# Performance work log

Measured on AMD Instinct MI355X. Metric: run time of the kernel, lower is better.

## Reference

```python
import jax, jax.numpy as jnp
import numpy as np

B, S, W, D, T = 64, 512, 384, 768, 21


def setup_inputs() -> dict:
    key = jax.random.key(0)
    ks = jax.random.split(key, 8)
    hidden_states = jax.random.normal(ks[0], (B, S, D), dtype=jnp.float32)  # BERT last_hidden_state
    word_maps = jnp.sort(jax.random.randint(ks[1], (B, W), 0, S), axis=1)  # first-subword index per word
    tags = jax.random.randint(ks[2], (B, W), 0, T)
    word_mask = jnp.ones((B, W), dtype=bool)  # torchcrf requires mask[:,0] all on
    W_tag = jax.random.normal(ks[3], (T, D), dtype=jnp.float32) * 0.02  # hidden2tag weight
    b_tag = jnp.zeros((T,), dtype=jnp.float32)
    start_trans = jax.random.uniform(ks[4], (T,), minval=-0.1, maxval=0.1)
    end_trans = jax.random.uniform(ks[5], (T,), minval=-0.1, maxval=0.1)
    trans = jax.random.uniform(ks[6], (T, T), minval=-0.1, maxval=0.1)
    return dict(hidden_states=hidden_states, W_tag=W_tag, b_tag=b_tag,
                start_trans=start_trans, end_trans=end_trans, trans=trans,
                word_maps=word_maps, tags=tags, word_mask=word_mask)


def reference(hidden_states, W_tag, b_tag, start_trans, end_trans, trans,
              word_maps, tags, word_mask):
    # --- ragged subword -> word gather (vectorized form of the python loop) ---
    word_feats = jnp.take_along_axis(hidden_states, word_maps[:, :, None], axis=1)  # [B,W,D]
    # dropout is identity in eval / deterministic reference
    emissions = jnp.einsum('bwd,td->bwt', word_feats, W_tag) + b_tag  # [B,W,T]

    maskf = word_mask.astype(emissions.dtype)
    bidx = jnp.arange(tags.shape[0])

    # --- CRF numerator: score of the given tag sequence ---
    emit_sc = jnp.take_along_axis(emissions, tags[:, :, None], axis=2)[..., 0]  # [B,W]
    trans_sc = trans[tags[:, :-1], tags[:, 1:]]                                  # [B,W-1]
    num = start_trans[tags[:, 0]] + emit_sc[:, 0]
    num = num + jnp.sum((trans_sc + emit_sc[:, 1:]) * maskf[:, 1:], axis=1)
    lengths = word_mask.sum(axis=1)
    last_tags = jnp.take_along_axis(tags, (lengths - 1)[:, None], axis=1)[:, 0]
    num = num + end_trans[last_tags]

    # --- CRF denominator: log partition via forward recurrence (scan over time) ---
    def step(score, xm):
        em_t, m_t = xm  # [B,T], [B]
        nxt = jax.nn.logsumexp(score[:, :, None] + trans[None, :, :] + em_t[:, None, :], axis=1)
        return jnp.where(m_t[:, None], nxt, score), None

    score0 = start_trans[None, :] + emissions[:, 0]  # [B,T]
    score, _ = jax.lax.scan(step, score0,
                            (jnp.swapaxes(emissions[:, 1:], 0, 1), word_mask[:, 1:].T))
    log_z = jax.nn.logsumexp(score + end_trans[None, :], axis=1)  # [B]

    llh = num - log_z
    return -jnp.mean(llh)  # reduction='mean', negated
```

## Files before the change

kernel.cpp:

```cpp
#include <hip/hip_runtime.h>
#include <math.h>

#define BB 64
#define SS 512
#define WW 384
#define DD 768
#define TT 21
#define ROWS (BB*WW)
#define EMSTRIDE (WW*TT)
#define NCH 32
#define CLEN 12
#define PSTRIDE 24
#define PMATSZ (TT*PSTRIDE)
#define PTSZ (PSTRIDE*PSTRIDE)
#define LN32 3.4657359027997265f

typedef short   bf16x8 __attribute__((ext_vector_type(8)));
typedef float   f32x4  __attribute__((ext_vector_type(4)));
union FragU { bf16x8 v; unsigned u[4]; };

__device__ __forceinline__ unsigned pack_bf16(unsigned lo, unsigned hi) {
    return __builtin_amdgcn_perm(hi, lo, 0x07060302);
}

__global__ __launch_bounds__(256) void emissions_kernel(
    const float* __restrict__ hidden, const int* __restrict__ word_maps,
    const float* __restrict__ W_tag, const float* __restrict__ b_tag,
    float* __restrict__ em, float* __restrict__ out)
{
    __shared__ __align__(16) unsigned short Bs[24 * 2 * 4 * 16 * 8];
    __shared__ __align__(16) float Sred[2][64][8];
    __shared__ int rowoff[32];

    const int tid = threadIdx.x;
    const int rowBase = blockIdx.x * 32;

    if (blockIdx.x == 0 && tid == 0) out[0] = 0.0f;

    if (tid < 32) {
        int row = rowBase + tid;
        int b = row / WW;
        int w = row - b * WW;
        rowoff[tid] = b * SS + word_maps[b * WW + w];
    }

    for (int i = tid; i < TT * (DD / 4); i += 256) {
        int t = i / (DD / 4), q = i - t * (DD / 4);
        int k  = q * 4;
        int ks = k >> 5, quad = (k >> 3) & 3, e = k & 7;
        int nt = t >> 4, l16 = t & 15;
        float4 wv = *(const float4*)&W_tag[t * DD + k];
        int off = ((ks * 2 + nt) * 4 + quad) * 128 + l16 * 8 + e;
        *(unsigned*)&Bs[off]     = pack_bf16(__float_as_uint(wv.x), __float_as_uint(wv.y));
        *(unsigned*)&Bs[off + 2] = pack_bf16(__float_as_uint(wv.z), __float_as_uint(wv.w));
    }
    __syncthreads();

    const int wv_  = tid >> 6;
    const int rt   = wv_ >> 1;
    const int h    = wv_ & 1;
    const int lane = tid & 63;
    const int l16  = lane & 15;
    const int quad = lane >> 4;

    const float* abase = hidden + (size_t)rowoff[rt * 16 + l16] * DD
                                + h * (DD / 2) + quad * 8;
    const unsigned short* bbase = Bs + quad * 128 + l16 * 8 + h * 12 * 1024;

    f32x4 acc0 = {}, acc1 = {};

    float4 A0[4], A1[4];
    #pragma unroll
    for (int p = 0; p < 4; ++p) {
        A0[p] = *(const float4*)(abase + p * 32);
        A1[p] = *(const float4*)(abase + p * 32 + 4);
    }
    bf16x8 b0c = *(const bf16x8*)(bbase);
    bf16x8 b1c = *(const bf16x8*)(bbase + 512);

    #pragma unroll
    for (int ks = 0; ks < 12; ++ks) {
        bf16x8 b0n = b0c, b1n = b1c;
        if (ks < 11) {
            b0n = *(const bf16x8*)(bbase + (ks + 1) * 1024);
            b1n = *(const bf16x8*)(bbase + (ks + 1) * 1024 + 512);
        }
        FragU a;
        a.u[0] = pack_bf16(__float_as_uint(A0[ks & 3].x), __float_as_uint(A0[ks & 3].y));
        a.u[1] = pack_bf16(__float_as_uint(A0[ks & 3].z), __float_as_uint(A0[ks & 3].w));
        a.u[2] = pack_bf16(__float_as_uint(A1[ks & 3].x), __float_as_uint(A1[ks & 3].y));
        a.u[3] = pack_bf16(__float_as_uint(A1[ks & 3].z), __float_as_uint(A1[ks & 3].w));
        if (ks < 8) {
            A0[ks & 3] = *(const float4*)(abase + (ks + 4) * 32);
            A1[ks & 3] = *(const float4*)(abase + (ks + 4) * 32 + 4);
        }
        acc0 = __builtin_amdgcn_mfma_f32_16x16x32_bf16(a.v, b0c, acc0, 0, 0, 0);
        acc1 = __builtin_amdgcn_mfma_f32_16x16x32_bf16(a.v, b1c, acc1, 0, 0, 0);
        b0c = b0n; b1c = b1n;
    }

    if (h == 1) {
        #pragma unroll
        for (int r = 0; r < 4; ++r) {
            Sred[rt][lane][r]     = acc0[r];
            Sred[rt][lane][r + 4] = acc1[r];
        }
    }
    __syncthreads();

    if (h == 0) {
        #pragma unroll
        for (int r = 0; r < 4; ++r) {
            acc0[r] += Sred[rt][lane][r];
            acc1[r] += Sred[rt][lane][r + 4];
        }
        int rbase = rowBase + rt * 16 + quad * 4;
        {
            float bt = b_tag[l16];
            #pragma unroll
            for (int r = 0; r < 4; ++r)
                em[(size_t)(rbase + r) * TT + l16] = acc0[r] + bt;
        }
        if (16 + l16 < TT) {
            float bt = b_tag[16 + l16];
            #pragma unroll
            for (int r = 0; r < 4; ++r)
                em[(size_t)(rbase + r) * TT + 16 + l16] = acc1[r] + bt;
        }
    }
}

__global__ __launch_bounds__(256, 1) void chunk_kernel(
    const float* __restrict__ em, const float* __restrict__ trans,
    float* __restrict__ Pmat)
{
    __shared__ __align__(16) float Es[PTSZ];
    __shared__ __align__(16) float Pbuf[4][2][PMATSZ];
    __shared__ __align__(16) float gem[4][CLEN * PSTRIDE];

    const int tid  = threadIdx.x;
    const int wid  = tid >> 6;
    const int lane = tid & 63;
    const int id   = blockIdx.x * 4 + wid;
    const int b    = id / NCH;
    const int c    = id - b * NCH;
    const int s0   = 1 + c * CLEN;
    const int n    = (c == NCH - 1) ? (WW - s0) : CLEN;

    for (int idx = tid; idx < PTSZ; idx += 256) {
        int k = idx / PSTRIDE, j = idx - k * PSTRIDE;
        Es[idx] = (k < TT && j < TT) ? __expf(trans[k * TT + j]) * 0.03125f : 0.f;
    }

    int i3r = lane / 6;
    const int jg  = lane - i3r * 6;
    const bool active = (i3r < 7) && (jg < 6);
    const int i3 = (i3r < 7) ? i3r : 6;
    const int jbase = (jg < 6 ? jg : 5) * 4;

    for (int idx = lane; idx < n * PSTRIDE; idx += 64) {
        int tt = idx / PSTRIDE, j = idx - tt * PSTRIDE;
        float g = 1.0f;
        if (j < TT) g = __expf(em[((size_t)b * WW + (s0 + tt)) * TT + j]);
        gem[wid][idx] = g;
    }
    __syncthreads();

    {
        float4 g = *(const float4*)&gem[wid][jbase];
        #pragma unroll
        for (int r = 0; r < 3; ++r) {
            int i = i3 * 3 + r;
            float4 e = *(const float4*)&Es[i * PSTRIDE + jbase];
            float4 v = make_float4(e.x * g.x, e.y * g.y, e.z * g.z, e.w * g.w);
            if (active) *(float4*)&Pbuf[wid][0][i * PSTRIDE + jbase] = v;
        }
    }

    int pp = 0;
    for (int tt = 1; tt < n; ++tt) {
        float acc[3][4];
        #pragma unroll
        for (int r = 0; r < 3; ++r)
            #pragma unroll
            for (int q = 0; q < 4; ++q) acc[r][q] = 0.f;

        const float* Pc = &Pbuf[wid][pp][0];
        #pragma unroll
        for (int kb = 0; kb < 6; ++kb) {
            float4 p0 = *(const float4*)&Pc[(i3 * 3 + 0) * PSTRIDE + kb * 4];
            float4 p1 = *(const float4*)&Pc[(i3 * 3 + 1) * PSTRIDE + kb * 4];
            float4 p2 = *(const float4*)&Pc[(i3 * 3 + 2) * PSTRIDE + kb * 4];
            #pragma unroll
            for (int kk = 0; kk < 4; ++kk) {
                const int k = kb * 4 + kk;
                float4 e = *(const float4*)&Es[k * PSTRIDE + jbase];
                float a = (kk == 0) ? p0.x : (kk == 1) ? p0.y : (kk == 2) ? p0.z : p0.w;
                float bv= (kk == 0) ? p1.x : (kk == 1) ? p1.y : (kk == 2) ? p1.z : p1.w;
                float cv= (kk == 0) ? p2.x : (kk == 1) ? p2.y : (kk == 2) ? p2.z : p2.w;
                acc[0][0] = fmaf(a, e.x, acc[0][0]); acc[0][1] = fmaf(a, e.y, acc[0][1]);
                acc[0][2] = fmaf(a, e.z, acc[0][2]); acc[0][3] = fmaf(a, e.w, acc[0][3]);
                acc[1][0] = fmaf(bv, e.x, acc[1][0]); acc[1][1] = fmaf(bv, e.y, acc[1][1]);
                acc[1][2] = fmaf(bv, e.z, acc[1][2]); acc[1][3] = fmaf(bv, e.w, acc[1][3]);
                acc[2][0] = fmaf(cv, e.x, acc[2][0]); acc[2][1] = fmaf(cv, e.y, acc[2][1]);
                acc[2][2] = fmaf(cv, e.z, acc[2][2]); acc[2][3] = fmaf(cv, e.w, acc[2][3]);
            }
        }
        float4 g = *(const float4*)&gem[wid][tt * PSTRIDE + jbase];
        if (active) {
            #pragma unroll
            for (int r = 0; r < 3; ++r) {
                float4 v = make_float4(acc[r][0] * g.x, acc[r][1] * g.y,
                                       acc[r][2] * g.z, acc[r][3] * g.w);
                *(float4*)&Pbuf[wid][1 - pp][(i3 * 3 + r) * PSTRIDE + jbase] = v;
            }
        }
        pp ^= 1;
    }

    float* dst = Pmat + (size_t)id * PTSZ;
    const float* Pf = &Pbuf[wid][pp][0];
    for (int idx = lane; idx < PTSZ; idx += 64) {
        int j = idx / PSTRIDE, i = idx - j * PSTRIDE;
        dst[idx] = (i < TT) ? Pf[i * PSTRIDE + j] : 0.f;
    }
}

__device__ __forceinline__ float lane_bcast(float v, int l) {
    return __uint_as_float(__builtin_amdgcn_readlane(__float_as_uint(v), l));
}

__global__ __launch_bounds__(64, 1) void combine_kernel(
    const float* __restrict__ Pmat, const float* __restrict__ em,
    const int* __restrict__ tags, const float* __restrict__ start_trans,
    const float* __restrict__ end_trans, const float* __restrict__ trans,
    float* __restrict__ out)
{
    const int b = blockIdx.x;
    const int j = threadIdx.x;
    const bool act = (j < TT);
    const int jc = act ? j : (TT - 1);
    const float* emb = em + (size_t)b * EMSTRIDE;

    float s0v = start_trans[jc] + emb[jc];
    float M = act ? s0v : -1e30f;
    #pragma unroll
    for (int o = 32; o > 0; o >>= 1) M = fmaxf(M, __shfl_xor(M, o));
    float sig = act ? __expf(s0v - M) : 0.0f;

    const float* Pb = Pmat + (size_t)b * NCH * PTSZ + jc * PSTRIDE;
    float4 a0 = *(const float4*)&Pb[0];
    float4 a1 = *(const float4*)&Pb[4];
    float4 a2 = *(const float4*)&Pb[8];
    float4 a3 = *(const float4*)&Pb[12];
    float4 a4 = *(const float4*)&Pb[16];
    float  a5 = Pb[20];

    for (int c = 0; c < NCH; ++c) {
        int cn = (c + 1 < NCH) ? c + 1 : c;
        const float* Pn = Pb + (size_t)cn * PTSZ;
        float4 n0 = *(const float4*)&Pn[0];
        float4 n1 = *(const float4*)&Pn[4];
        float4 n2 = *(const float4*)&Pn[8];
        float4 n3 = *(const float4*)&Pn[12];
        float4 n4 = *(const float4*)&Pn[16];
        float  n5 = Pn[20];

        float col[TT];
        col[0]=a0.x;  col[1]=a0.y;  col[2]=a0.z;  col[3]=a0.w;
        col[4]=a1.x;  col[5]=a1.y;  col[6]=a1.z;  col[7]=a1.w;
        col[8]=a2.x;  col[9]=a2.y;  col[10]=a2.z; col[11]=a2.w;
        col[12]=a3.x; col[13]=a3.y; col[14]=a3.z; col[15]=a3.w;
        col[16]=a4.x; col[17]=a4.y; col[18]=a4.z; col[19]=a4.w;
        col[20]=a5;
        float p0 = 0.f, p1 = 0.f, p2 = 0.f;
        #pragma unroll
        for (int i = 0; i < TT; i += 3) {
            p0 = fmaf(lane_bcast(sig, i    ), col[i    ], p0);
            p1 = fmaf(lane_bcast(sig, i + 1), col[i + 1], p1);
            p2 = fmaf(lane_bcast(sig, i + 2), col[i + 2], p2);
        }
        float v = act ? (p0 + p1 + p2) : 0.0f;
        float m = v;
        #pragma unroll
        for (int o = 32; o > 0; o >>= 1) m = fmaxf(m, __shfl_xor(m, o));
        int nst = (c == NCH - 1) ? (WW - (1 + c * CLEN)) : CLEN;
        M += __logf(m) + (float)nst * LN32;
        sig = v / m;

        a0 = n0; a1 = n1; a2 = n2; a3 = n3; a4 = n4; a5 = n5;
    }

    float fin = (act && sig > 0.f) ? (M + __logf(sig) + end_trans[jc]) : -1e30f;
    float mm = fin;
    #pragma unroll
    for (int o = 32; o > 0; o >>= 1) mm = fmaxf(mm, __shfl_xor(mm, o));
    float pe = __expf(fin - mm);
    float ssum = pe;
    #pragma unroll
    for (int o = 32; o > 0; o >>= 1) ssum += __shfl_xor(ssum, o);
    float lz = mm + __logf(ssum);

    const int* tb = tags + b * WW;
    float part = 0.f;
    for (int w = j; w < WW; w += 64) {
        int tw = tb[w];
        float e = emb[w * TT + tw];
        float tsc = (w == 0) ? start_trans[tw] : trans[tb[w - 1] * TT + tw];
        part += tsc + e;
    }
    #pragma unroll
    for (int o = 32; o > 0; o >>= 1) part += __shfl_xor(part, o);

    if (j == 0) {
        float num = part + end_trans[tb[WW - 1]];
        atomicAdd(out, -(num - lz) * (1.0f / BB));
    }
}

extern "C" void kernel_launch(void* const* d_in, const int* in_sizes, int n_in,
                              void* d_out, int out_size, void* d_ws, size_t ws_size,
                              hipStream_t stream) {
    const float* hidden      = (const float*)d_in[0];
    const float* W_tag       = (const float*)d_in[1];
    const float* b_tag       = (const float*)d_in[2];
    const float* start_trans = (const float*)d_in[3];
    const float* end_trans   = (const float*)d_in[4];
    const float* trans       = (const float*)d_in[5];
    const int*   word_maps   = (const int*)  d_in[6];
    const int*   tags        = (const int*)  d_in[7];

    float* out  = (float*)d_out;
    float* em   = (float*)d_ws;
    float* Pmat = (float*)d_ws + (size_t)ROWS * TT;

    emissions_kernel<<<ROWS / 32, 256, 0, stream>>>(hidden, word_maps, W_tag, b_tag, em, out);
    chunk_kernel<<<BB * NCH / 4, 256, 0, stream>>>(em, trans, Pmat);
    combine_kernel<<<BB, 64, 0, stream>>>(Pmat, em, tags, start_trans, end_trans, trans, out);
}
```

Before: 195.2 us.

## Cache transition tile in registers, pad LDS stride, deepen combine prefetch

In the chunk kernel, the 24 float4 columns of the scaled transition matrix are loaded into registers once instead of being re-read from LDS every step. The LDS row stride is padded from 24 to 28 floats to reduce bank conflicts, and launch bounds now allow two blocks per CU. The combine kernel prefetches four chunk matrices ahead instead of one, to hide global-load latency in the serial merge chain. The costs are much higher register pressure (96 extra VGPRs for Er) that may conflict with the 2-block occupancy hint, and more registers in the combine kernel.

```diff
diff --git a/kernel.cpp b/kernel.cpp
--- a/kernel.cpp
+++ b/kernel.cpp
@@ -11,7 +11,7 @@
 #define NCH 32
 #define CLEN 12
 #define PSTRIDE 24
-#define PMATSZ (TT*PSTRIDE)
+#define LSTR 28
 #define PTSZ (PSTRIDE*PSTRIDE)
 #define LN32 3.4657359027997265f
 
@@ -130,13 +130,13 @@
     }
 }
 
-__global__ __launch_bounds__(256, 1) void chunk_kernel(
+__global__ __launch_bounds__(256, 2) void chunk_kernel(
     const float* __restrict__ em, const float* __restrict__ trans,
     float* __restrict__ Pmat)
 {
-    __shared__ __align__(16) float Es[PTSZ];
-    __shared__ __align__(16) float Pbuf[4][2][PMATSZ];
-    __shared__ __align__(16) float gem[4][CLEN * PSTRIDE];
+    __shared__ __align__(16) float Es[24 * LSTR];
+    __shared__ __align__(16) float Pbuf[4][2][21 * LSTR];
+    __shared__ __align__(16) float gem[4][CLEN * LSTR];
 
     const int tid  = threadIdx.x;
     const int wid  = tid >> 6;
@@ -147,8 +147,8 @@
     const int s0   = 1 + c * CLEN;
     const int n    = (c == NCH - 1) ? (WW - s0) : CLEN;
 
-    for (int idx = tid; idx < PTSZ; idx += 256) {
-        int k = idx / PSTRIDE, j = idx - k * PSTRIDE;
+    for (int idx = tid; idx < 24 * LSTR; idx += 256) {
+        int k = idx / LSTR, j = idx - k * LSTR;
         Es[idx] = (k < TT && j < TT) ? __expf(trans[k * TT + j]) * 0.03125f : 0.f;
     }
 
@@ -158,22 +158,27 @@
     const int i3 = (i3r < 7) ? i3r : 6;
     const int jbase = (jg < 6 ? jg : 5) * 4;
 
-    for (int idx = lane; idx < n * PSTRIDE; idx += 64) {
-        int tt = idx / PSTRIDE, j = idx - tt * PSTRIDE;
+    for (int idx = lane; idx < n * LSTR; idx += 64) {
+        int tt = idx / LSTR, j = idx - tt * LSTR;
         float g = 1.0f;
         if (j < TT) g = __expf(em[((size_t)b * WW + (s0 + tt)) * TT + j]);
         gem[wid][idx] = g;
     }
     __syncthreads();
 
+    float4 Er[24];
+    #pragma unroll
+    for (int k = 0; k < 24; ++k)
+        Er[k] = *(const float4*)&Es[k * LSTR + jbase];
+
     {
         float4 g = *(const float4*)&gem[wid][jbase];
         #pragma unroll
         for (int r = 0; r < 3; ++r) {
             int i = i3 * 3 + r;
-            float4 e = *(const float4*)&Es[i * PSTRIDE + jbase];
+            float4 e = *(const float4*)&Es[i * LSTR + jbase];
             float4 v = make_float4(e.x * g.x, e.y * g.y, e.z * g.z, e.w * g.w);
-            if (active) *(float4*)&Pbuf[wid][0][i * PSTRIDE + jbase] = v;
+            if (active) *(float4*)&Pbuf[wid][0][i * LSTR + jbase] = v;
         }
     }
 
@@ -188,13 +193,12 @@
         const float* Pc = &Pbuf[wid][pp][0];
         #pragma unroll
         for (int kb = 0; kb < 6; ++kb) {
-            float4 p0 = *(const float4*)&Pc[(i3 * 3 + 0) * PSTRIDE + kb * 4];
-            float4 p1 = *(const float4*)&Pc[(i3 * 3 + 1) * PSTRIDE + kb * 4];
-            float4 p2 = *(const float4*)&Pc[(i3 * 3 + 2) * PSTRIDE + kb * 4];
+            float4 p0 = *(const float4*)&Pc[(i3 * 3 + 0) * LSTR + kb * 4];
+            float4 p1 = *(const float4*)&Pc[(i3 * 3 + 1) * LSTR + kb * 4];
+            float4 p2 = *(const float4*)&Pc[(i3 * 3 + 2) * LSTR + kb * 4];
             #pragma unroll
             for (int kk = 0; kk < 4; ++kk) {
-                const int k = kb * 4 + kk;
-                float4 e = *(const float4*)&Es[k * PSTRIDE + jbase];
+                float4 e = Er[kb * 4 + kk];
                 float a = (kk == 0) ? p0.x : (kk == 1) ? p0.y : (kk == 2) ? p0.z : p0.w;
                 float bv= (kk == 0) ? p1.x : (kk == 1) ? p1.y : (kk == 2) ? p1.z : p1.w;
                 float cv= (kk == 0) ? p2.x : (kk == 1) ? p2.y : (kk == 2) ? p2.z : p2.w;
@@ -206,13 +210,13 @@
                 acc[2][2] = fmaf(cv, e.z, acc[2][2]); acc[2][3] = fmaf(cv, e.w, acc[2][3]);
             }
         }
-        float4 g = *(const float4*)&gem[wid][tt * PSTRIDE + jbase];
+        float4 g = *(const float4*)&gem[wid][tt * LSTR + jbase];
         if (active) {
             #pragma unroll
             for (int r = 0; r < 3; ++r) {
                 float4 v = make_float4(acc[r][0] * g.x, acc[r][1] * g.y,
                                        acc[r][2] * g.z, acc[r][3] * g.w);
-                *(float4*)&Pbuf[wid][1 - pp][(i3 * 3 + r) * PSTRIDE + jbase] = v;
+                *(float4*)&Pbuf[wid][1 - pp][(i3 * 3 + r) * LSTR + jbase] = v;
             }
         }
         pp ^= 1;
@@ -222,13 +226,42 @@
     const float* Pf = &Pbuf[wid][pp][0];
     for (int idx = lane; idx < PTSZ; idx += 64) {
         int j = idx / PSTRIDE, i = idx - j * PSTRIDE;
-        dst[idx] = (i < TT) ? Pf[i * PSTRIDE + j] : 0.f;
+        dst[idx] = (i < TT) ? Pf[i * LSTR + j] : 0.f;
     }
 }
 
 __device__ __forceinline__ float lane_bcast(float v, int l) {
     return __uint_as_float(__builtin_amdgcn_readlane(__float_as_uint(v), l));
 }
+
+#define LOADC(q0,q1,q2,q3,q4,q5,cc) { \
+    const float* Pp = Pb + (size_t)(cc) * PTSZ; \
+    q0 = *(const float4*)&Pp[0];  q1 = *(const float4*)&Pp[4]; \
+    q2 = *(const float4*)&Pp[8];  q3 = *(const float4*)&Pp[12]; \
+    q4 = *(const float4*)&Pp[16]; q5 = Pp[20]; }
+
+#define MERGE(c_, q0,q1,q2,q3,q4,q5) { \
+    float col[TT]; \
+    col[0]=q0.x;  col[1]=q0.y;  col[2]=q0.z;  col[3]=q0.w; \
+    col[4]=q1.x;  col[5]=q1.y;  col[6]=q1.z;  col[7]=q1.w; \
+    col[8]=q2.x;  col[9]=q2.y;  col[10]=q2.z; col[11]=q2.w; \
+    col[12]=q3.x; col[13]=q3.y; col[14]=q3.z; col[15]=q3.w; \
+    col[16]=q4.x; col[17]=q4.y; col[18]=q4.z; col[19]=q4.w; \
+    col[20]=q5; \
+    float p0 = 0.f, p1 = 0.f, p2 = 0.f; \
+    _Pragma("unroll") \
+    for (int i = 0; i < TT; i += 3) { \
+        p0 = fmaf(lane_bcast(sig, i    ), col[i    ], p0); \
+        p1 = fmaf(lane_bcast(sig, i + 1), col[i + 1], p1); \
+        p2 = fmaf(lane_bcast(sig, i + 2), col[i + 2], p2); \
+    } \
+    float v = act ? (p0 + p1 + p2) : 0.0f; \
+    float m = v; \
+    _Pragma("unroll") \
+    for (int o = 32; o > 0; o >>= 1) m = fmaxf(m, __shfl_xor(m, o)); \
+    int nst = ((c_) == NCH - 1) ? (WW - (1 + (c_) * CLEN)) : CLEN; \
+    M += __logf(m) + (float)nst * LN32; \
+    sig = v / m; }
 
 __global__ __launch_bounds__(64, 1) void combine_kernel(
     const float* __restrict__ Pmat, const float* __restrict__ em,
@@ -241,6 +274,16 @@
     const bool act = (j < TT);
     const int jc = act ? j : (TT - 1);
     const float* emb = em + (size_t)b * EMSTRIDE;
+    const float* Pb = Pmat + (size_t)b * NCH * PTSZ + jc * PSTRIDE;
+
+    float4 A0,A1,A2,A3,A4; float A5;
+    float4 B0,B1,B2,B3,B4; float B5;
+    float4 C0,C1,C2,C3,C4; float C5;
+    float4 D0,D1,D2,D3,D4; float D5;
+    LOADC(A0,A1,A2,A3,A4,A5, 0);
+    LOADC(B0,B1,B2,B3,B4,B5, 1);
+    LOADC(C0,C1,C2,C3,C4,C5, 2);
+    LOADC(D0,D1,D2,D3,D4,D5, 3);
 
     float s0v = start_trans[jc] + emb[jc];
     float M = act ? s0v : -1e30f;
@@ -248,47 +291,15 @@
     for (int o = 32; o > 0; o >>= 1) M = fmaxf(M, __shfl_xor(M, o));
     float sig = act ? __expf(s0v - M) : 0.0f;
 
-    const float* Pb = Pmat + (size_t)b * NCH * PTSZ + jc * PSTRIDE;
-    float4 a0 = *(const float4*)&Pb[0];
-    float4 a1 = *(const float4*)&Pb[4];
-    float4 a2 = *(const float4*)&Pb[8];
-    float4 a3 = *(const float4*)&Pb[12];
-    float4 a4 = *(const float4*)&Pb[16];
-    float  a5 = Pb[20];
-
-    for (int c = 0; c < NCH; ++c) {
-        int cn = (c + 1 < NCH) ? c + 1 : c;
-        const float* Pn = Pb + (size_t)cn * PTSZ;
-        float4 n0 = *(const float4*)&Pn[0];
-        float4 n1 = *(const float4*)&Pn[4];
-        float4 n2 = *(const float4*)&Pn[8];
-        float4 n3 = *(const float4*)&Pn[12];
-        float4 n4 = *(const float4*)&Pn[16];
-        float  n5 = Pn[20];
-
-        float col[TT];
-        col[0]=a0.x;  col[1]=a0.y;  col[2]=a0.z;  col[3]=a0.w;
-        col[4]=a1.x;  col[5]=a1.y;  col[6]=a1.z;  col[7]=a1.w;
-        col[8]=a2.x;  col[9]=a2.y;  col[10]=a2.z; col[11]=a2.w;
-        col[12]=a3.x; col[13]=a3.y; col[14]=a3.z; col[15]=a3.w;
-        col[16]=a4.x; col[17]=a4.y; col[18]=a4.z; col[19]=a4.w;
-        col[20]=a5;
-        float p0 = 0.f, p1 = 0.f, p2 = 0.f;
-        #pragma unroll
-        for (int i = 0; i < TT; i += 3) {
-            p0 = fmaf(lane_bcast(sig, i    ), col[i    ], p0);
-            p1 = fmaf(lane_bcast(sig, i + 1), col[i + 1], p1);
-            p2 = fmaf(lane_bcast(sig, i + 2), col[i + 2], p2);
-        }
-        float v = act ? (p0 + p1 + p2) : 0.0f;
-        float m = v;
-        #pragma unroll
-        for (int o = 32; o > 0; o >>= 1) m = fmaxf(m, __shfl_xor(m, o));
-        int nst = (c == NCH - 1) ? (WW - (1 + c * CLEN)) : CLEN;
-        M += __logf(m) + (float)nst * LN32;
-        sig = v / m;
-
-        a0 = n0; a1 = n1; a2 = n2; a3 = n3; a4 = n4; a5 = n5;
+    for (int c = 0; c < NCH; c += 4) {
+        MERGE(c,     A0,A1,A2,A3,A4,A5);
+        if (c + 4 < NCH) LOADC(A0,A1,A2,A3,A4,A5, c + 4);
+        MERGE(c + 1, B0,B1,B2,B3,B4,B5);
+        if (c + 5 < NCH) LOADC(B0,B1,B2,B3,B4,B5, c + 5);
+        MERGE(c + 2, C0,C1,C2,C3,C4,C5);
+        if (c + 6 < NCH) LOADC(C0,C1,C2,C3,C4,C5, c + 6);
+        MERGE(c + 3, D0,D1,D2,D3,D4,D5);
+        if (c + 7 < NCH) LOADC(D0,D1,D2,D3,D4,D5, c + 7);
     }
 
     float fin = (act && sig > 0.f) ? (M + __logf(sig) + end_trans[jc]) : -1e30f;
@@ -303,6 +314,7 @@
 
     const int* tb = tags + b * WW;
     float part = 0.f;
+    #pragma unroll
     for (int w = j; w < WW; w += 64) {
         int tw = tb[w];
         float e = emb[w * TT + tw];
```

Result: no change. 196.9 us (+0.8%).
